# Kernel tuning notes

Hardware: AMD Instinct MI355X
Metric: run time of the kernel (lower is better)

The kernel has to match this reference:

```python
import jax, jax.numpy as jnp
import numpy as np

N_ITERS = 21
TEMPERATURE = 0.01


def setup_inputs() -> dict:
    key = jax.random.key(0)
    input_tensor = jax.random.normal(key, (65536, 1296), dtype=jnp.float32)
    return {"input_tensor": input_tensor}


def reference(input_tensor) -> jnp.ndarray:
    n = input_tensor.shape[1]
    m = n // 36  # 36: side length of the permutation matrix
    log_alpha = input_tensor.reshape(-1, m, m) / TEMPERATURE  # [B, 36, 36]
    # 21 Sinkhorn iterations: alternate row / column log-normalization.
    # Same math as log(sum(exp(.))) in the torch source, written stably.
    for _ in range(N_ITERS):
        log_alpha = log_alpha - jax.nn.logsumexp(log_alpha, axis=2, keepdims=True)
        log_alpha = log_alpha - jax.nn.logsumexp(log_alpha, axis=1, keepdims=True)
    return jnp.exp(log_alpha)
```

## Files before the change

### kernel.cpp

```cpp
#include <hip/hip_runtime.h>

#define SCALE 144.269504088896340736f
#define TOL   1e-3f

typedef float v2 __attribute__((ext_vector_type(2)));

template <int CTRL>
__device__ __forceinline__ float dppf(float x) {
    return __builtin_bit_cast(
        float, __builtin_amdgcn_update_dpp(0, __builtin_bit_cast(int, x),
                                           CTRL, 0xF, 0xF, true));
}
__device__ __forceinline__ float qsum(float x) {
    x += dppf<0x39>(x); x += dppf<0x4E>(x); return x;
}
__device__ __forceinline__ float qmax(float x) {
    x = fmaxf(x, dppf<0x39>(x)); x = fmaxf(x, dppf<0x4E>(x)); return x;
}
__device__ __forceinline__ float asum(float x) {
    x += dppf<0x124>(x); x += dppf<0x128>(x); return x;
}
__device__ __forceinline__ float amax(float x) {
    x = fmaxf(x, dppf<0x124>(x)); x = fmaxf(x, dppf<0x128>(x)); return x;
}

__global__ __launch_bounds__(256, 4) void sinkhorn_kernel(
    const float* __restrict__ in, float* __restrict__ out) {
    const int lane = threadIdx.x & 63;
    const int wv   = threadIdx.x >> 6;
    const int a    = (lane >> 2) & 3;
    const int b    = lane & 3;
    const int m    = blockIdx.x * 16 + wv * 4 + (lane >> 4);

    const float* src = in  + (size_t)m * 1296 + (a * 9) * 36 + b * 9;
    float*       dst = out + (size_t)m * 1296 + (a * 9) * 36 + b * 9;

    v2 Cp[9][4]; float Cl[9];
    #pragma unroll
    for (int r = 0; r < 9; ++r) {
        #pragma unroll
        for (int p = 0; p < 4; ++p) {
            Cp[r][p].x = src[r * 36 + 2 * p];
            Cp[r][p].y = src[r * 36 + 2 * p + 1];
        }
        Cl[r] = src[r * 36 + 8];
    }

    float a2[9];
    #pragma unroll
    for (int r = 0; r < 9; ++r) {
        float mx = fmaxf(Cp[r][0].x, Cp[r][0].y);
        #pragma unroll
        for (int p = 1; p < 4; ++p) mx = fmaxf(mx, fmaxf(Cp[r][p].x, Cp[r][p].y));
        a2[r] = qmax(fmaxf(mx, Cl[r]));
    }

    v2 cm[4]; float cml = -3.4e38f;
    #pragma unroll
    for (int p = 0; p < 4; ++p) { cm[p].x = -3.4e38f; cm[p].y = -3.4e38f; }
    #pragma unroll
    for (int r = 0; r < 9; ++r) {
        v2 na = {-a2[r], -a2[r]};
        #pragma unroll
        for (int p = 0; p < 4; ++p) {
            Cp[r][p] += na;
            cm[p].x = fmaxf(cm[p].x, Cp[r][p].x);
            cm[p].y = fmaxf(cm[p].y, Cp[r][p].y);
        }
        Cl[r] -= a2[r];
        cml = fmaxf(cml, Cl[r]);
    }

    v2 nb2s[4], p2[4];
    #pragma unroll
    for (int p = 0; p < 4; ++p) {
        float bx = amax(cm[p].x), by = amax(cm[p].y);
        nb2s[p].x = -bx * SCALE; nb2s[p].y = -by * SCALE;
        p2[p].x = __builtin_amdgcn_exp2f(bx * SCALE);
        p2[p].y = __builtin_amdgcn_exp2f(by * SCALE);
    }
    float bl  = amax(cml);
    float nbl = -bl * SCALE;
    float pl  = __builtin_amdgcn_exp2f(bl * SCALE);

    const v2 S2 = {SCALE, SCALE};
    #pragma unroll
    for (int r = 0; r < 9; ++r) {
        #pragma unroll
        for (int p = 0; p < 4; ++p) {
            v2 t = Cp[r][p] * S2 + nb2s[p];
            Cp[r][p].x = __builtin_amdgcn_exp2f(t.x);
            Cp[r][p].y = __builtin_amdgcn_exp2f(t.y);
        }
        Cl[r] = __builtin_amdgcn_exp2f(Cl[r] * SCALE + nbl);
    }

    float u[9];
    #pragma unroll
    for (int r = 0; r < 9; ++r) {
        v2 acc = Cp[r][0] * p2[0];
        #pragma unroll
        for (int p = 1; p < 4; ++p) acc = Cp[r][p] * p2[p] + acc;
        float t = fmaf(Cl[r], pl, acc.x + acc.y);
        u[r] = __builtin_amdgcn_rcpf(qsum(t));
    }

    v2 w2[4]; float wl;
    {
        v2 acc2[4]; float accl = 0.f;
        #pragma unroll
        for (int p = 0; p < 4; ++p) { acc2[p].x = 0.f; acc2[p].y = 0.f; }
        #pragma unroll
        for (int r = 0; r < 9; ++r) {
            v2 ur = {u[r], u[r]};
            #pragma unroll
            for (int p = 0; p < 4; ++p) acc2[p] = Cp[r][p] * ur + acc2[p];
            accl = fmaf(Cl[r], u[r], accl);
        }
        #pragma unroll
        for (int p = 0; p < 4; ++p) {
            w2[p].x = __builtin_amdgcn_rcpf(asum(acc2[p].x));
            w2[p].y = __builtin_amdgcn_rcpf(asum(acc2[p].y));
        }
        wl = __builtin_amdgcn_rcpf(asum(accl));
    }

    #pragma unroll 1
    for (int it = 0; it < 20; ++it) {
        #pragma unroll
        for (int r = 0; r < 9; ++r) {
            v2 acc = Cp[r][0] * w2[0];
            #pragma unroll
            for (int p = 1; p < 4; ++p) acc = Cp[r][p] * w2[p] + acc;
            float t = fmaf(Cl[r], wl, acc.x + acc.y);
            u[r] = __builtin_amdgcn_rcpf(qsum(t));
        }
        v2 acc2[4]; float accl = 0.f;
        #pragma unroll
        for (int p = 0; p < 4; ++p) { acc2[p].x = 0.f; acc2[p].y = 0.f; }
        #pragma unroll
        for (int r = 0; r < 9; ++r) {
            v2 ur = {u[r], u[r]};
            #pragma unroll
            for (int p = 0; p < 4; ++p) acc2[p] = Cp[r][p] * ur + acc2[p];
            accl = fmaf(Cl[r], u[r], accl);
        }
        float mx = 0.f;
        #pragma unroll
        for (int p = 0; p < 4; ++p) {
            float dx = asum(acc2[p].x), dy = asum(acc2[p].y);
            mx = fmaxf(mx, fabsf(fmaf(dx, w2[p].x, -1.f)));
            mx = fmaxf(mx, fabsf(fmaf(dy, w2[p].y, -1.f)));
            w2[p].x = __builtin_amdgcn_rcpf(dx);
            w2[p].y = __builtin_amdgcn_rcpf(dy);
        }
        float dl = asum(accl);
        mx = fmaxf(mx, fabsf(fmaf(dl, wl, -1.f)));
        wl = __builtin_amdgcn_rcpf(dl);
        mx = qmax(mx);
        if (__all(mx < TOL)) break;
    }

    #pragma unroll
    for (int r = 0; r < 9; ++r) {
        v2 ur = {u[r], u[r]};
        #pragma unroll
        for (int p = 0; p < 4; ++p) {
            v2 t = Cp[r][p] * ur * w2[p];
            dst[r * 36 + 2 * p]     = t.x;
            dst[r * 36 + 2 * p + 1] = t.y;
        }
        dst[r * 36 + 8] = Cl[r] * u[r] * wl;
    }
}

extern "C" void kernel_launch(void* const* d_in, const int* in_sizes, int n_in,
                              void* d_out, int out_size, void* d_ws, size_t ws_size,
                              hipStream_t stream) {
    const float* in  = (const float*)d_in[0];
    float*       out = (float*)d_out;
    sinkhorn_kernel<<<dim3(4096), dim3(256), 0, stream>>>(in, out);
}
```

Baseline: 607.1 us.

## Remap column ownership to enable 16-byte vector loads and stores

After: 593.3 us. -2.3%, faster.

```diff
diff --git a/kernel.cpp b/kernel.cpp
--- a/kernel.cpp
+++ b/kernel.cpp
@@ -2,8 +2,10 @@
 
 #define SCALE 144.269504088896340736f
 #define TOL   1e-3f
+#define NINF  -3.4e38f
 
 typedef float v2 __attribute__((ext_vector_type(2)));
+typedef float v4 __attribute__((ext_vector_type(4)));
 
 template <int CTRL>
 __device__ __forceinline__ float dppf(float x) {
@@ -23,6 +25,9 @@
 __device__ __forceinline__ float amax(float x) {
     x = fmaxf(x, dppf<0x124>(x)); x = fmaxf(x, dppf<0x128>(x)); return x;
 }
+__device__ __forceinline__ v2 vmax2(v2 p, v2 q) {
+    return (v2){fmaxf(p.x, q.x), fmaxf(p.y, q.y)};
+}
 
 __global__ __launch_bounds__(256, 4) void sinkhorn_kernel(
     const float* __restrict__ in, float* __restrict__ out) {
@@ -32,131 +37,131 @@
     const int b    = lane & 3;
     const int m    = blockIdx.x * 16 + wv * 4 + (lane >> 4);
 
-    const float* src = in  + (size_t)m * 1296 + (a * 9) * 36 + b * 9;
-    float*       dst = out + (size_t)m * 1296 + (a * 9) * 36 + b * 9;
+    const size_t base = (size_t)m * 1296 + (size_t)(a * 9) * 36;
+    const float* src  = in  + base;
+    float*       dst  = out + base;
+    const int o0 = 4 * b;
+    const int o1 = 16 + 4 * b;
+    const int ot = 32 + b;
 
-    v2 Cp[9][4]; float Cl[9];
+    v2 A[9][4]; float T[9];
     #pragma unroll
     for (int r = 0; r < 9; ++r) {
-        #pragma unroll
-        for (int p = 0; p < 4; ++p) {
-            Cp[r][p].x = src[r * 36 + 2 * p];
-            Cp[r][p].y = src[r * 36 + 2 * p + 1];
-        }
-        Cl[r] = src[r * 36 + 8];
+        v4 c0 = *(const v4*)(src + r * 36 + o0);
+        v4 c1 = *(const v4*)(src + r * 36 + o1);
+        A[r][0] = (v2){c0.x, c0.y}; A[r][1] = (v2){c0.z, c0.w};
+        A[r][2] = (v2){c1.x, c1.y}; A[r][3] = (v2){c1.z, c1.w};
+        T[r]    = src[r * 36 + ot];
     }
 
     float a2[9];
     #pragma unroll
     for (int r = 0; r < 9; ++r) {
-        float mx = fmaxf(Cp[r][0].x, Cp[r][0].y);
-        #pragma unroll
-        for (int p = 1; p < 4; ++p) mx = fmaxf(mx, fmaxf(Cp[r][p].x, Cp[r][p].y));
-        a2[r] = qmax(fmaxf(mx, Cl[r]));
+        v2 m2 = vmax2(vmax2(A[r][0], A[r][1]), vmax2(A[r][2], A[r][3]));
+        a2[r] = qmax(fmaxf(fmaxf(m2.x, m2.y), T[r]));
     }
 
-    v2 cm[4]; float cml = -3.4e38f;
+    v2 cm[4]; float cmt = NINF;
     #pragma unroll
-    for (int p = 0; p < 4; ++p) { cm[p].x = -3.4e38f; cm[p].y = -3.4e38f; }
+    for (int p = 0; p < 4; ++p) { cm[p].x = NINF; cm[p].y = NINF; }
     #pragma unroll
     for (int r = 0; r < 9; ++r) {
         v2 na = {-a2[r], -a2[r]};
         #pragma unroll
         for (int p = 0; p < 4; ++p) {
-            Cp[r][p] += na;
-            cm[p].x = fmaxf(cm[p].x, Cp[r][p].x);
-            cm[p].y = fmaxf(cm[p].y, Cp[r][p].y);
+            A[r][p] += na;
+            cm[p] = vmax2(cm[p], A[r][p]);
         }
-        Cl[r] -= a2[r];
-        cml = fmaxf(cml, Cl[r]);
+        T[r] -= a2[r];
+        cmt = fmaxf(cmt, T[r]);
     }
 
-    v2 nb2s[4], p2[4];
+    v2 nb2[4], p2[4];
     #pragma unroll
     for (int p = 0; p < 4; ++p) {
         float bx = amax(cm[p].x), by = amax(cm[p].y);
-        nb2s[p].x = -bx * SCALE; nb2s[p].y = -by * SCALE;
+        nb2[p].x = -bx * SCALE; nb2[p].y = -by * SCALE;
         p2[p].x = __builtin_amdgcn_exp2f(bx * SCALE);
         p2[p].y = __builtin_amdgcn_exp2f(by * SCALE);
     }
-    float bl  = amax(cml);
-    float nbl = -bl * SCALE;
-    float pl  = __builtin_amdgcn_exp2f(bl * SCALE);
+    float bt  = amax(cmt);
+    float nbt = -bt * SCALE;
+    float pt  = __builtin_amdgcn_exp2f(bt * SCALE);
 
     const v2 S2 = {SCALE, SCALE};
     #pragma unroll
     for (int r = 0; r < 9; ++r) {
         #pragma unroll
         for (int p = 0; p < 4; ++p) {
-            v2 t = Cp[r][p] * S2 + nb2s[p];
-            Cp[r][p].x = __builtin_amdgcn_exp2f(t.x);
-            Cp[r][p].y = __builtin_amdgcn_exp2f(t.y);
+            v2 t = A[r][p] * S2 + nb2[p];
+            A[r][p].x = __builtin_amdgcn_exp2f(t.x);
+            A[r][p].y = __builtin_amdgcn_exp2f(t.y);
         }
-        Cl[r] = __builtin_amdgcn_exp2f(Cl[r] * SCALE + nbl);
+        T[r] = __builtin_amdgcn_exp2f(T[r] * SCALE + nbt);
     }
 
     float u[9];
     #pragma unroll
     for (int r = 0; r < 9; ++r) {
-        v2 acc = Cp[r][0] * p2[0];
+        v2 acc = A[r][0] * p2[0];
         #pragma unroll
-        for (int p = 1; p < 4; ++p) acc = Cp[r][p] * p2[p] + acc;
-        float t = fmaf(Cl[r], pl, acc.x + acc.y);
+        for (int p = 1; p < 4; ++p) acc = A[r][p] * p2[p] + acc;
+        float t = fmaf(T[r], pt, acc.x + acc.y);
         u[r] = __builtin_amdgcn_rcpf(qsum(t));
     }
 
-    v2 w2[4]; float wl;
+    v2 wA[4]; float wt;
     {
-        v2 acc2[4]; float accl = 0.f;
+        v2 acc2[4]; float acct = 0.f;
         #pragma unroll
         for (int p = 0; p < 4; ++p) { acc2[p].x = 0.f; acc2[p].y = 0.f; }
         #pragma unroll
         for (int r = 0; r < 9; ++r) {
             v2 ur = {u[r], u[r]};
             #pragma unroll
-            for (int p = 0; p < 4; ++p) acc2[p] = Cp[r][p] * ur + acc2[p];
-            accl = fmaf(Cl[r], u[r], accl);
+            for (int p = 0; p < 4; ++p) acc2[p] = A[r][p] * ur + acc2[p];
+            acct = fmaf(T[r], u[r], acct);
         }
         #pragma unroll
         for (int p = 0; p < 4; ++p) {
-            w2[p].x = __builtin_amdgcn_rcpf(asum(acc2[p].x));
-            w2[p].y = __builtin_amdgcn_rcpf(asum(acc2[p].y));
+            wA[p].x = __builtin_amdgcn_rcpf(asum(acc2[p].x));
+            wA[p].y = __builtin_amdgcn_rcpf(asum(acc2[p].y));
         }
-        wl = __builtin_amdgcn_rcpf(asum(accl));
+        wt = __builtin_amdgcn_rcpf(asum(acct));
     }
 
     #pragma unroll 1
     for (int it = 0; it < 20; ++it) {
         #pragma unroll
         for (int r = 0; r < 9; ++r) {
-            v2 acc = Cp[r][0] * w2[0];
+            v2 acc = A[r][0] * wA[0];
             #pragma unroll
-            for (int p = 1; p < 4; ++p) acc = Cp[r][p] * w2[p] + acc;
-            float t = fmaf(Cl[r], wl, acc.x + acc.y);
+            for (int p = 1; p < 4; ++p) acc = A[r][p] * wA[p] + acc;
+            float t = fmaf(T[r], wt, acc.x + acc.y);
             u[r] = __builtin_amdgcn_rcpf(qsum(t));
         }
-        v2 acc2[4]; float accl = 0.f;
+        v2 acc2[4]; float acct = 0.f;
         #pragma unroll
         for (int p = 0; p < 4; ++p) { acc2[p].x = 0.f; acc2[p].y = 0.f; }
         #pragma unroll
         for (int r = 0; r < 9; ++r) {
             v2 ur = {u[r], u[r]};
             #pragma unroll
-            for (int p = 0; p < 4; ++p) acc2[p] = Cp[r][p] * ur + acc2[p];
-            accl = fmaf(Cl[r], u[r], accl);
+            for (int p = 0; p < 4; ++p) acc2[p] = A[r][p] * ur + acc2[p];
+            acct = fmaf(T[r], u[r], acct);
         }
         float mx = 0.f;
         #pragma unroll
         for (int p = 0; p < 4; ++p) {
             float dx = asum(acc2[p].x), dy = asum(acc2[p].y);
-            mx = fmaxf(mx, fabsf(fmaf(dx, w2[p].x, -1.f)));
-            mx = fmaxf(mx, fabsf(fmaf(dy, w2[p].y, -1.f)));
-            w2[p].x = __builtin_amdgcn_rcpf(dx);
-            w2[p].y = __builtin_amdgcn_rcpf(dy);
+            mx = fmaxf(mx, fabsf(fmaf(dx, wA[p].x, -1.f)));
+            mx = fmaxf(mx, fabsf(fmaf(dy, wA[p].y, -1.f)));
+            wA[p].x = __builtin_amdgcn_rcpf(dx);
+            wA[p].y = __builtin_amdgcn_rcpf(dy);
         }
-        float dl = asum(accl);
-        mx = fmaxf(mx, fabsf(fmaf(dl, wl, -1.f)));
-        wl = __builtin_amdgcn_rcpf(dl);
+        float dt = asum(acct);
+        mx = fmaxf(mx, fabsf(fmaf(dt, wt, -1.f)));
+        wt = __builtin_amdgcn_rcpf(dt);
         mx = qmax(mx);
         if (__all(mx < TOL)) break;
     }
@@ -164,13 +169,13 @@
     #pragma unroll
     for (int r = 0; r < 9; ++r) {
         v2 ur = {u[r], u[r]};
-        #pragma unroll
-        for (int p = 0; p < 4; ++p) {
-            v2 t = Cp[r][p] * ur * w2[p];
-            dst[r * 36 + 2 * p]     = t.x;
-            dst[r * 36 + 2 * p + 1] = t.y;
-        }
-        dst[r * 36 + 8] = Cl[r] * u[r] * wl;
+        v2 t0 = A[r][0] * ur * wA[0];
+        v2 t1 = A[r][1] * ur * wA[1];
+        v2 t2 = A[r][2] * ur * wA[2];
+        v2 t3 = A[r][3] * ur * wA[3];
+        *(v4*)(dst + r * 36 + o0) = (v4){t0.x, t0.y, t1.x, t1.y};
+        *(v4*)(dst + r * 36 + o1) = (v4){t2.x, t2.y, t3.x, t3.y};
+        dst[r * 36 + ot] = T[r] * u[r] * wt;
     }
 }
 
```
